# Kernel optimization log

Hardware: AMD Instinct MI355X
Metric: run time of the kernel (lower is better)

Reference implementation:

```python
import jax, jax.numpy as jnp
import numpy as np

E = 100  # embed_size


def _forward_sentence(noun_emb, subj_cube, obj_cube, words, vs, vo, vt):
    # words: [W] noun ids; vs/vo: [N,2]; vt: [N,3]
    word_sum = noun_emb[words].sum(axis=0)  # [E]
    # gather verb matrices (rows of E*E) in the original cat order
    verb_mats = jnp.concatenate([
        subj_cube[vs[:, 0]],
        obj_cube[vo[:, 0]],
        subj_cube[vt[:, 0]],
        obj_cube[vt[:, 0]],
    ], axis=0).reshape(-1, E, E)  # [4N, E, E]
    arg_vecs = jnp.concatenate([
        noun_emb[vs[:, 1]],
        noun_emb[vo[:, 1]],
        noun_emb[vt[:, 1]],
        noun_emb[vt[:, 2]],
    ], axis=0)  # [4N, E]
    # batched matrix-vector product then reduce over all edges
    verb_arg_sum = jnp.einsum('nij,nj->i', verb_mats, arg_vecs)  # [E]
    return word_sum + verb_arg_sum


def setup_inputs() -> dict:
    key = jax.random.key(0)
    ks = jax.random.split(key, 16)
    n_nouns, n_verbs, hidden = 100000, 5000, 300
    inp = {
        'words1': jax.random.randint(ks[0], (50000,), 0, n_nouns),
        'verb_subj1': jax.random.randint(ks[1], (5000, 2), 0, n_verbs),
        'verb_obj1': jax.random.randint(ks[2], (5000, 2), 0, n_verbs),
        'verb_trans1': jax.random.randint(ks[3], (5000, 3), 0, n_verbs),
        'words2': jax.random.randint(ks[4], (50000,), 0, n_nouns),
        'verb_subj2': jax.random.randint(ks[5], (5000, 2), 0, n_verbs),
        'verb_obj2': jax.random.randint(ks[6], (5000, 2), 0, n_verbs),
        'verb_trans2': jax.random.randint(ks[7], (5000, 3), 0, n_verbs),
        'noun_emb': jax.random.normal(ks[8], (n_nouns, E), jnp.float32) * 0.1,
        'subj_cube': jax.random.normal(ks[9], (n_verbs, E * E), jnp.float32) * 0.02,
        'obj_cube': jax.random.normal(ks[10], (n_verbs, E * E), jnp.float32) * 0.02,
        'W_h': jax.random.normal(ks[11], (hidden, 4 * E), jnp.float32) * 0.05,
        'b_h': jax.random.normal(ks[12], (hidden,), jnp.float32) * 0.05,
        'W_o': jax.random.normal(ks[13], (3, hidden), jnp.float32) * 0.05,
        'b_o': jax.random.normal(ks[14], (3,), jnp.float32) * 0.05,
    }
    return inp


def reference(words1, verb_subj1, verb_obj1, verb_trans1,
              words2, verb_subj2, verb_obj2, verb_trans2,
              noun_emb, subj_cube, obj_cube, W_h, b_h, W_o, b_o):
    emb1 = _forward_sentence(noun_emb, subj_cube, obj_cube, words1, verb_subj1, verb_obj1, verb_trans1)
    emb2 = _forward_sentence(noun_emb, subj_cube, obj_cube, words2, verb_subj2, verb_obj2, verb_trans2)
    mult_dist = emb1 * emb2
    abs_dist = jnp.abs(emb1 - emb2)
    vec_dist = jnp.concatenate([emb1, emb2, mult_dist, abs_dist], axis=0)  # [4E]
    h = jax.nn.sigmoid(vec_dist @ W_h.T + b_h)  # [hidden]
    out = jax.nn.log_softmax(h @ W_o.T + b_o, axis=-1)  # [3]
    return out
```

## Files before the change

### kernel.cpp

```cpp
#include <hip/hip_runtime.h>
#include <math.h>

#define E 100
#define NV 5000
#define NPART 64
#define CAP 16


__global__ void init_kernel(int* __restrict__ count, float* __restrict__ partial) {
    int p = blockIdx.x * blockDim.x + threadIdx.x;
    if (p < 4 * NV) count[p] = 0;
    if (p < NPART * 2 * E) partial[p] = 0.f;
}

__global__ void bucket_build_kernel(const int* __restrict__ vs1, const int* __restrict__ vo1,
                                    const int* __restrict__ vt1,
                                    const int* __restrict__ vs2, const int* __restrict__ vo2,
                                    const int* __restrict__ vt2,
                                    int* __restrict__ count, int* __restrict__ bucket) {
    int p = blockIdx.x * blockDim.x + threadIdx.x;
    if (p >= 40000) return;
    int sent = p / 20000;
    int r = p - sent * 20000;
    int kind = r / 5000;
    int idx = r - kind * 5000;
    const int* vs = sent ? vs2 : vs1;
    const int* vo = sent ? vo2 : vo1;
    const int* vt = sent ? vt2 : vt1;
    int verb, arg, cube;
    if (kind == 0)      { verb = vs[idx * 2]; arg = vs[idx * 2 + 1]; cube = 0; }
    else if (kind == 1) { verb = vo[idx * 2]; arg = vo[idx * 2 + 1]; cube = 1; }
    else if (kind == 2) { verb = vt[idx * 3]; arg = vt[idx * 3 + 1]; cube = 0; }
    else                { verb = vt[idx * 3]; arg = vt[idx * 3 + 2]; cube = 1; }
    int slot = (cube * 2 + sent) * NV + verb;
    int pos = atomicAdd(&count[slot], 1);
    if (pos < CAP) bucket[slot * CAP + pos] = arg;
}

__global__ void build_A_kernel(const int* __restrict__ count, const int* __restrict__ bucket,
                               const float* __restrict__ noun_emb, float* __restrict__ A) {
    int p = blockIdx.x * blockDim.x + threadIdx.x;
    if (p >= 4 * NV * 25) return;
    int slot = p / 25, c = p - (p / 25) * 25;
    int n = count[slot]; if (n > CAP) n = CAP;
    const int4* b4 = (const int4*)(bucket + slot * CAP);
    int4 q0 = b4[0], q1 = b4[1], q2 = b4[2], q3 = b4[3];
    int ids[16] = {q0.x,q0.y,q0.z,q0.w, q1.x,q1.y,q1.z,q1.w,
                   q2.x,q2.y,q2.z,q2.w, q3.x,q3.y,q3.z,q3.w};
    const float4* ne4 = (const float4*)noun_emb;
    float ax = 0.f, ay = 0.f, az = 0.f, aw = 0.f;
    #pragma unroll
    for (int j = 0; j < CAP; j++)
        if (j < n) {
            float4 v = ne4[ids[j] * 25 + c];
            ax += v.x; ay += v.y; az += v.z; aw += v.w;
        }
    ((float4*)A)[p] = make_float4(ax, ay, az, aw);
}

__global__ __launch_bounds__(512) void word_sum_kernel(const int* __restrict__ w1,
                                                       const int* __restrict__ w2,
                                                       const float* __restrict__ noun_emb,
                                                       float* __restrict__ partial) {
    __shared__ int wid[400];
    __shared__ float wred[E];
    int b = blockIdx.x;
    int sent = b / 125;
    int cb = b - sent * 125;
    const int* words = sent ? w2 : w1;
    int t = threadIdx.x;
    if (t < 400) wid[t] = words[cb * 400 + t];
    if (t >= 400 && t < 500) wred[t - 400] = 0.f;
    __syncthreads();
    if (t < 500) {
        int wl = t / 25, k = t - (t / 25) * 25;
        const float4* ne4 = (const float4*)noun_emb;
        float ax = 0.f, ay = 0.f, az = 0.f, aw = 0.f;
        #pragma unroll
        for (int j = 0; j < 20; j++) {
            float4 v = ne4[wid[wl * 20 + j] * 25 + k];
            ax += v.x; ay += v.y; az += v.z; aw += v.w;
        }
        atomicAdd(&wred[k * 4 + 0], ax);
        atomicAdd(&wred[k * 4 + 1], ay);
        atomicAdd(&wred[k * 4 + 2], az);
        atomicAdd(&wred[k * 4 + 3], aw);
    }
    __syncthreads();
    if (t < 100) atomicAdd(&partial[((b & (NPART - 1)) * 2 + sent) * E + t], wred[t]);
}

__global__ __launch_bounds__(256, 4) void cube_stream_kernel(const float* __restrict__ subj,
                                                             const float* __restrict__ obj,
                                                             const float* __restrict__ A,
                                                             float* __restrict__ partial) {
    int r = blockIdx.x * 256 + threadIdx.x;
    if (r >= 2 * NV * E) return;
    int cube = r / (NV * E);
    int rem = r - cube * (NV * E);
    int v = rem / E, i = rem - v * E;
    const float4* row = (const float4*)(cube ? obj : subj) + (size_t)rem * 25;
    const float4* x1  = (const float4*)A + ((size_t)(cube * 2 + 0) * NV + v) * 25;
    const float4* x2  = (const float4*)A + ((size_t)(cube * 2 + 1) * NV + v) * 25;

    float a1e = 0.f, a1o = 0.f, a2e = 0.f, a2o = 0.f;
    #pragma unroll
    for (int k = 0; k < 24; k += 2) {
        float4 m0 = row[k],   m1 = row[k + 1];
        float4 p0 = x1[k],    p1 = x1[k + 1];
        float4 q0 = x2[k],    q1 = x2[k + 1];
        a1e += m0.x * p0.x + m0.y * p0.y + m0.z * p0.z + m0.w * p0.w;
        a1o += m1.x * p1.x + m1.y * p1.y + m1.z * p1.z + m1.w * p1.w;
        a2e += m0.x * q0.x + m0.y * q0.y + m0.z * q0.z + m0.w * q0.w;
        a2o += m1.x * q1.x + m1.y * q1.y + m1.z * q1.z + m1.w * q1.w;
    }
    {
        float4 m0 = row[24];
        float4 p0 = x1[24], q0 = x2[24];
        a1e += m0.x * p0.x + m0.y * p0.y + m0.z * p0.z + m0.w * p0.w;
        a2e += m0.x * q0.x + m0.y * q0.y + m0.z * q0.z + m0.w * q0.w;
    }
    int sl = (blockIdx.x & (NPART - 1)) * 2;
    atomicAdd(&partial[(sl + 0) * E + i], a1e + a1o);
    atomicAdd(&partial[(sl + 1) * E + i], a2e + a2o);
}

__global__ __launch_bounds__(512) void hidden_kernel(const float* __restrict__ partial,
                                                     const float* __restrict__ W_h,
                                                     const float* __restrict__ b_h,
                                                     float* __restrict__ hbuf) {
    __shared__ float vds[4 * E];
    int t = threadIdx.x;
    if (t < 200) {
        int s = t / 100, i = t - (t / 100) * 100;
        float sum = 0.f;
        #pragma unroll 8
        for (int p = 0; p < NPART; p++) sum += partial[(p * 2 + s) * E + i];
        vds[s * E + i] = sum;
    }
    __syncthreads();
    if (t < E) {
        float e1 = vds[t], e2 = vds[E + t];
        vds[2 * E + t] = e1 * e2;
        vds[3 * E + t] = fabsf(e1 - e2);
    }
    __syncthreads();
    int wave = t >> 6, lane = t & 63;
    int h = blockIdx.x * 8 + wave;
    if (h < 300) {
        const float4* w4 = (const float4*)(W_h + (size_t)h * 4 * E);
        const float4* v4 = (const float4*)vds;
        float4 w = w4[lane], v = v4[lane];
        float acc = w.x * v.x + w.y * v.y + w.z * v.z + w.w * v.w;
        if (lane < 36) {
            float4 w2 = w4[lane + 64], v2 = v4[lane + 64];
            acc += w2.x * v2.x + w2.y * v2.y + w2.z * v2.z + w2.w * v2.w;
        }
        #pragma unroll
        for (int off = 32; off > 0; off >>= 1) acc += __shfl_down(acc, off);
        if (lane == 0) hbuf[h] = 1.f / (1.f + expf(-(acc + b_h[h])));
    }
}

__global__ __launch_bounds__(512) void out_kernel(const float* __restrict__ hbuf,
                                                  const float* __restrict__ W_o,
                                                  const float* __restrict__ b_o,
                                                  float* __restrict__ out) {
    __shared__ float hs[300];
    __shared__ float o[3];
    int t = threadIdx.x;
    if (t < 300) hs[t] = hbuf[t];
    __syncthreads();
    int wave = t >> 6, lane = t & 63;
    if (wave < 3) {
        float acc = 0.f;
        #pragma unroll
        for (int j = 0; j < 5; j++) {
            int h = lane + j * 64;
            if (h < 300) acc += W_o[wave * 300 + h] * hs[h];
        }
        #pragma unroll
        for (int off = 32; off > 0; off >>= 1) acc += __shfl_down(acc, off);
        if (lane == 0) o[wave] = acc + b_o[wave];
    }
    __syncthreads();
    if (t == 0) {
        float m = fmaxf(o[0], fmaxf(o[1], o[2]));
        float l = logf(expf(o[0] - m) + expf(o[1] - m) + expf(o[2] - m)) + m;
        out[0] = o[0] - l;
        out[1] = o[1] - l;
        out[2] = o[2] - l;
    }
}

extern "C" void kernel_launch(void* const* d_in, const int* in_sizes, int n_in,
                              void* d_out, int out_size, void* d_ws, size_t ws_size,
                              hipStream_t stream) {
    const int* words1 = (const int*)d_in[0];
    const int* vs1    = (const int*)d_in[1];
    const int* vo1    = (const int*)d_in[2];
    const int* vt1    = (const int*)d_in[3];
    const int* words2 = (const int*)d_in[4];
    const int* vs2    = (const int*)d_in[5];
    const int* vo2    = (const int*)d_in[6];
    const int* vt2    = (const int*)d_in[7];
    const float* noun_emb = (const float*)d_in[8];
    const float* subj     = (const float*)d_in[9];
    const float* obj      = (const float*)d_in[10];
    const float* W_h      = (const float*)d_in[11];
    const float* b_h      = (const float*)d_in[12];
    const float* W_o      = (const float*)d_in[13];
    const float* b_o      = (const float*)d_in[14];
    float* out = (float*)d_out;

    int*   count   = (int*)d_ws;
    int*   bucket  = count + 4 * NV;
    float* A       = (float*)(bucket + 4 * NV * CAP);
    float* partial = A + 4 * NV * E;
    float* hbuf    = partial + NPART * 2 * E;

    init_kernel<<<(4 * NV + 255) / 256, 256, 0, stream>>>(count, partial);
    bucket_build_kernel<<<(40000 + 255) / 256, 256, 0, stream>>>(
        vs1, vo1, vt1, vs2, vo2, vt2, count, bucket);
    build_A_kernel<<<(4 * NV * 25 + 255) / 256, 256, 0, stream>>>(count, bucket, noun_emb, A);
    word_sum_kernel<<<250, 512, 0, stream>>>(words1, words2, noun_emb, partial);
    cube_stream_kernel<<<(2 * NV * E + 255) / 256, 256, 0, stream>>>(subj, obj, A, partial);
    hidden_kernel<<<38, 512, 0, stream>>>(partial, W_h, b_h, hbuf);
    out_kernel<<<1, 512, 0, stream>>>(hbuf, W_o, b_o, out);
}
```

Before: 542.3 us.

## Stream verb matrices as coalesced per-verb panels with shared-memory row reduction

Replaces the one-thread-per-row cube streaming kernel with one block per verb matrix. Each thread reads consecutive float4s of the 100x100 panel, so global loads are fully coalesced; before, each thread walked its own 400-byte row, giving strided access. The argument vectors are staged once in shared memory, and the per-row sums are reduced through a shared-memory panel before one atomic per row. This cuts atomics per row but adds two block barriers and 10000 blocks of 512 threads, 12 of which sit idle.

Result: faster. 458.6 us (-15.4%).

```diff
diff --git a/kernel.cpp b/kernel.cpp
--- a/kernel.cpp
+++ b/kernel.cpp
@@ -90,39 +90,51 @@
     if (t < 100) atomicAdd(&partial[((b & (NPART - 1)) * 2 + sent) * E + t], wred[t]);
 }
 
-__global__ __launch_bounds__(256, 4) void cube_stream_kernel(const float* __restrict__ subj,
-                                                             const float* __restrict__ obj,
-                                                             const float* __restrict__ A,
-                                                             float* __restrict__ partial) {
-    int r = blockIdx.x * 256 + threadIdx.x;
-    if (r >= 2 * NV * E) return;
-    int cube = r / (NV * E);
-    int rem = r - cube * (NV * E);
-    int v = rem / E, i = rem - v * E;
-    const float4* row = (const float4*)(cube ? obj : subj) + (size_t)rem * 25;
-    const float4* x1  = (const float4*)A + ((size_t)(cube * 2 + 0) * NV + v) * 25;
-    const float4* x2  = (const float4*)A + ((size_t)(cube * 2 + 1) * NV + v) * 25;
-
-    float a1e = 0.f, a1o = 0.f, a2e = 0.f, a2o = 0.f;
-    #pragma unroll
-    for (int k = 0; k < 24; k += 2) {
-        float4 m0 = row[k],   m1 = row[k + 1];
-        float4 p0 = x1[k],    p1 = x1[k + 1];
-        float4 q0 = x2[k],    q1 = x2[k + 1];
-        a1e += m0.x * p0.x + m0.y * p0.y + m0.z * p0.z + m0.w * p0.w;
-        a1o += m1.x * p1.x + m1.y * p1.y + m1.z * p1.z + m1.w * p1.w;
-        a2e += m0.x * q0.x + m0.y * q0.y + m0.z * q0.z + m0.w * q0.w;
-        a2o += m1.x * q1.x + m1.y * q1.y + m1.z * q1.z + m1.w * q1.w;
-    }
-    {
-        float4 m0 = row[24];
-        float4 p0 = x1[24], q0 = x2[24];
-        a1e += m0.x * p0.x + m0.y * p0.y + m0.z * p0.z + m0.w * p0.w;
-        a2e += m0.x * q0.x + m0.y * q0.y + m0.z * q0.z + m0.w * q0.w;
-    }
-    int sl = (blockIdx.x & (NPART - 1)) * 2;
-    atomicAdd(&partial[(sl + 0) * E + i], a1e + a1o);
-    atomicAdd(&partial[(sl + 1) * E + i], a2e + a2o);
+__global__ __launch_bounds__(512, 6) void verb_panel_kernel(const float* __restrict__ subj,
+                                                            const float* __restrict__ obj,
+                                                            const float* __restrict__ A,
+                                                            float* __restrict__ partial) {
+    __shared__ float4 xs[2][25];
+    __shared__ float  pl[2][E][25];
+
+    int b = blockIdx.x;
+    int cube = b / NV;
+    int v = b - cube * NV;
+    int t = threadIdx.x;
+
+    if (t < 50) {
+        int s = t / 25, c = t - (t / 25) * 25;
+        xs[s][c] = ((const float4*)A)[((size_t)(cube * 2 + s) * NV + v) * 25 + c];
+    }
+    __syncthreads();
+
+    if (t < 500) {
+        int c = t % 25, r0 = t / 25;
+        float4 x1 = xs[0][c], x2 = xs[1][c];
+        const float4* panel = (const float4*)(cube ? obj : subj) + (size_t)v * 2500;
+        float a1[5], a2[5];
+        #pragma unroll
+        for (int it = 0; it < 5; it++) {
+            float4 m = panel[it * 500 + t];
+            a1[it] = m.x * x1.x + m.y * x1.y + m.z * x1.z + m.w * x1.w;
+            a2[it] = m.x * x2.x + m.y * x2.y + m.z * x2.z + m.w * x2.w;
+        }
+        #pragma unroll
+        for (int it = 0; it < 5; it++) {
+            int row = it * 20 + r0;
+            pl[0][row][c] = a1[it];
+            pl[1][row][c] = a2[it];
+        }
+    }
+    __syncthreads();
+
+    if (t < 200) {
+        int s = t / 100, row = t - (t / 100) * 100;
+        float sum = 0.f;
+        #pragma unroll
+        for (int c = 0; c < 25; c++) sum += pl[s][row][c];
+        atomicAdd(&partial[((b & (NPART - 1)) * 2 + s) * E + row], sum);
+    }
 }
 
 __global__ __launch_bounds__(512) void hidden_kernel(const float* __restrict__ partial,
@@ -224,7 +236,7 @@
         vs1, vo1, vt1, vs2, vo2, vt2, count, bucket);
     build_A_kernel<<<(4 * NV * 25 + 255) / 256, 256, 0, stream>>>(count, bucket, noun_emb, A);
     word_sum_kernel<<<250, 512, 0, stream>>>(words1, words2, noun_emb, partial);
-    cube_stream_kernel<<<(2 * NV * E + 255) / 256, 256, 0, stream>>>(subj, obj, A, partial);
+    verb_panel_kernel<<<2 * NV, 512, 0, stream>>>(subj, obj, A, partial);
     hidden_kernel<<<38, 512, 0, stream>>>(partial, W_h, b_h, hbuf);
     out_kernel<<<1, 512, 0, stream>>>(hbuf, W_o, b_o, out);
 }
```

## Assign one wave per verb matrix with coalesced row loads and shuffle reduction

Applied to the files above, without the earlier changes.

Replaces the thread-per-row cube streaming kernel with a wave-per-verb kernel where each half-wave reads one 400-byte matrix row contiguously and reduces the dot products with shuffles. The argument vectors are loaded once per lane into registers. This targets the strided, uncoalesced per-thread row loads of the old kernel. In exchange, 7 of every 32 lanes sit idle and each row adds a shuffle reduction before the atomic adds.

New measurement: 500.2 us. 7.8% less time.

```diff
diff --git a/kernel.cpp b/kernel.cpp
--- a/kernel.cpp
+++ b/kernel.cpp
@@ -90,39 +90,46 @@
     if (t < 100) atomicAdd(&partial[((b & (NPART - 1)) * 2 + sent) * E + t], wred[t]);
 }
 
-__global__ __launch_bounds__(256, 4) void cube_stream_kernel(const float* __restrict__ subj,
-                                                             const float* __restrict__ obj,
-                                                             const float* __restrict__ A,
-                                                             float* __restrict__ partial) {
-    int r = blockIdx.x * 256 + threadIdx.x;
-    if (r >= 2 * NV * E) return;
-    int cube = r / (NV * E);
-    int rem = r - cube * (NV * E);
-    int v = rem / E, i = rem - v * E;
-    const float4* row = (const float4*)(cube ? obj : subj) + (size_t)rem * 25;
-    const float4* x1  = (const float4*)A + ((size_t)(cube * 2 + 0) * NV + v) * 25;
-    const float4* x2  = (const float4*)A + ((size_t)(cube * 2 + 1) * NV + v) * 25;
-
-    float a1e = 0.f, a1o = 0.f, a2e = 0.f, a2o = 0.f;
-    #pragma unroll
-    for (int k = 0; k < 24; k += 2) {
-        float4 m0 = row[k],   m1 = row[k + 1];
-        float4 p0 = x1[k],    p1 = x1[k + 1];
-        float4 q0 = x2[k],    q1 = x2[k + 1];
-        a1e += m0.x * p0.x + m0.y * p0.y + m0.z * p0.z + m0.w * p0.w;
-        a1o += m1.x * p1.x + m1.y * p1.y + m1.z * p1.z + m1.w * p1.w;
-        a2e += m0.x * q0.x + m0.y * q0.y + m0.z * q0.z + m0.w * q0.w;
-        a2o += m1.x * q1.x + m1.y * q1.y + m1.z * q1.z + m1.w * q1.w;
-    }
-    {
-        float4 m0 = row[24];
-        float4 p0 = x1[24], q0 = x2[24];
-        a1e += m0.x * p0.x + m0.y * p0.y + m0.z * p0.z + m0.w * p0.w;
-        a2e += m0.x * q0.x + m0.y * q0.y + m0.z * q0.z + m0.w * q0.w;
-    }
-    int sl = (blockIdx.x & (NPART - 1)) * 2;
-    atomicAdd(&partial[(sl + 0) * E + i], a1e + a1o);
-    atomicAdd(&partial[(sl + 1) * E + i], a2e + a2o);
+__global__ __launch_bounds__(256) void verb_wave_kernel(const float* __restrict__ subj,
+                                                        const float* __restrict__ obj,
+                                                        const float* __restrict__ A,
+                                                        float* __restrict__ partial) {
+    int tid  = blockIdx.x * 256 + threadIdx.x;
+    int wave = tid >> 6;
+    int lane = tid & 63;
+    int half = lane >> 5, cl = lane & 31;
+    int cube = wave / NV;
+    int v    = wave - cube * NV;
+    bool act = (cl < 25);
+
+    const float4* A4 = (const float4*)A;
+    float4 x1 = make_float4(0.f, 0.f, 0.f, 0.f), x2 = x1;
+    if (act) {
+        x1 = A4[((size_t)(cube * 2 + 0) * NV + v) * 25 + cl];
+        x2 = A4[((size_t)(cube * 2 + 1) * NV + v) * 25 + cl];
+    }
+    const float4* panel = (const float4*)(cube ? obj : subj) + (size_t)v * 2500;
+    int slice = (wave & (NPART - 1)) * 2;
+
+    #pragma unroll 2
+    for (int k = 0; k < 50; k++) {
+        int i = 2 * k + half;
+        float p1 = 0.f, p2 = 0.f;
+        if (act) {
+            float4 m = panel[i * 25 + cl];
+            p1 = m.x * x1.x + m.y * x1.y + m.z * x1.z + m.w * x1.w;
+            p2 = m.x * x2.x + m.y * x2.y + m.z * x2.z + m.w * x2.w;
+        }
+        #pragma unroll
+        for (int off = 16; off > 0; off >>= 1) {
+            p1 += __shfl_down(p1, off, 32);
+            p2 += __shfl_down(p2, off, 32);
+        }
+        if (cl == 0) {
+            atomicAdd(&partial[(slice + 0) * E + i], p1);
+            atomicAdd(&partial[(slice + 1) * E + i], p2);
+        }
+    }
 }
 
 __global__ __launch_bounds__(512) void hidden_kernel(const float* __restrict__ partial,
@@ -224,7 +231,7 @@
         vs1, vo1, vt1, vs2, vo2, vt2, count, bucket);
     build_A_kernel<<<(4 * NV * 25 + 255) / 256, 256, 0, stream>>>(count, bucket, noun_emb, A);
     word_sum_kernel<<<250, 512, 0, stream>>>(words1, words2, noun_emb, partial);
-    cube_stream_kernel<<<(2 * NV * E + 255) / 256, 256, 0, stream>>>(subj, obj, A, partial);
+    verb_wave_kernel<<<(2 * NV * 64 + 255) / 256, 256, 0, stream>>>(subj, obj, A, partial);
     hidden_kernel<<<38, 512, 0, stream>>>(partial, W_h, b_h, hbuf);
     out_kernel<<<1, 512, 0, stream>>>(hbuf, W_o, b_o, out);
 }
```
